# Optimization experiments

Measured on AMD Instinct MI355X. Metric: run time of the kernel, lower is better.

## Reference

```python
import jax, jax.numpy as jnp
import numpy as np

D_MODEL = 1024
D_STATE = 128
D_CONV = 4
EXPAND = 2
HEAD_DIM = 128
NGROUPS = 1
CHUNK = 256
D_INNER = EXPAND * D_MODEL          # 2048
HEADS = D_INNER // HEAD_DIM         # 16
D_IN_PROJ = 2 * D_INNER + 2 * NGROUPS * D_STATE + HEADS  # 4368
CONV_DIM = D_INNER + 2 * NGROUPS * D_STATE               # 2304
EPS = 1e-5


def setup_inputs() -> dict:
    key = jax.random.key(0)
    ks = jax.random.split(key, 10)
    B, L = 2, 2048
    u = jax.random.normal(ks[0], (B, L, D_MODEL), dtype=jnp.float32)
    in_proj_w = jax.random.normal(ks[1], (D_IN_PROJ, D_MODEL), dtype=jnp.float32) * 0.02
    conv_w = jax.random.normal(ks[2], (CONV_DIM, 1, D_CONV), dtype=jnp.float32) * 0.2
    conv_b = jnp.zeros((CONV_DIM,), dtype=jnp.float32)
    # dt_bias = inverse-softplus of dt sampled log-uniform in [dt_min, dt_max]
    dt = jnp.exp(jax.random.uniform(ks[3], (HEADS,)) * (np.log(0.1) - np.log(0.001)) + np.log(0.001))
    dt = jnp.clip(dt, 1e-4, None)
    dt_bias = (dt + jnp.log(-jnp.expm1(-dt))).astype(jnp.float32)
    A_log = jax.random.uniform(ks[4], (HEADS,), minval=np.log(0.001), maxval=np.log(0.999)).astype(jnp.float32)
    D_param = jax.random.uniform(ks[5], (HEADS,), minval=-0.5, maxval=0.5).astype(jnp.float32)
    norm_w = jnp.ones((D_INNER,), dtype=jnp.float32)
    out_proj_w = jax.random.normal(ks[6], (D_MODEL, D_INNER), dtype=jnp.float32) * 0.02
    out_proj_b = jnp.zeros((D_MODEL,), dtype=jnp.float32)
    return {"u": u, "in_proj_w": in_proj_w, "conv_w": conv_w, "conv_b": conv_b,
            "dt_bias": dt_bias, "A_log": A_log, "D_param": D_param,
            "norm_w": norm_w, "out_proj_w": out_proj_w, "out_proj_b": out_proj_b}


def _segsum_exp(a):
    # a: (..., T) -> exp of lower-triangular segment sums, (..., T, T)
    T = a.shape[-1]
    ac = jnp.cumsum(a, axis=-1)
    diff = ac[..., :, None] - ac[..., None, :]
    mask = jnp.tril(jnp.ones((T, T), dtype=bool))
    return jnp.where(mask, jnp.exp(jnp.where(mask, diff, 0.0)), 0.0)


def _ssd(xdt, dA, Bmat, Cmat):
    # xdt: (b,L,h,p) = x * dt ; dA: (b,L,h) = dt * A ; Bmat/Cmat: (b,L,n) (ngroups=1)
    b, L, h, p = xdt.shape
    nc, cs = L // CHUNK, CHUNK
    x_c = xdt.reshape(b, nc, cs, h, p)
    B_c = Bmat.reshape(b, nc, cs, -1)
    C_c = Cmat.reshape(b, nc, cs, -1)
    A_r = dA.reshape(b, nc, cs, h).transpose(0, 3, 1, 2)  # (b,h,nc,cs)
    Lmat = _segsum_exp(A_r)                               # (b,h,nc,cs,cs)
    Y_diag = jnp.einsum('bcin,bcjn,bhcij,bcjhp->bcihp', C_c, B_c, Lmat, x_c)
    A_cum = jnp.cumsum(A_r, axis=-1)                      # (b,h,nc,cs)
    decay_states = jnp.exp(A_cum[..., -1:] - A_cum)       # (b,h,nc,cs)
    states = jnp.einsum('bcin,bhci,bcihp->bchpn', B_c, decay_states, x_c)  # (b,nc,h,p,n)
    chunk_decay = jnp.exp(A_cum[..., -1])                 # (b,h,nc)

    def step(prev, inp):
        s, dec = inp  # s: (b,h,p,n), dec: (b,h)
        new = prev * dec[..., None, None] + s
        return new, prev  # emit state entering this chunk

    init = jnp.zeros((b, h, p, states.shape[-1]), dtype=xdt.dtype)
    _, prior = jax.lax.scan(step, init,
                            (states.transpose(1, 0, 2, 3, 4), chunk_decay.transpose(2, 0, 1)))
    prior = prior.transpose(1, 0, 2, 3, 4)                # (b,nc,h,p,n)
    state_decay_out = jnp.exp(A_cum)                      # (b,h,nc,cs)
    Y_off = jnp.einsum('bcin,bchpn,bhci->bcihp', C_c, prior, state_decay_out)
    return (Y_diag + Y_off).reshape(b, L, h, p)


def reference(u, in_proj_w, conv_w, conv_b, dt_bias, A_log, D_param, norm_w, out_proj_w, out_proj_b):
    b, L, _ = u.shape
    zxbcdt = u @ in_proj_w.T                              # (b,L,4368)
    z = zxbcdt[..., :D_INNER]
    xBC = zxbcdt[..., D_INNER:D_INNER + CONV_DIM]
    dt = zxbcdt[..., D_INNER + CONV_DIM:]                 # (b,L,H)
    dt = jax.nn.softplus(dt + dt_bias)
    # causal depthwise conv1d + SiLU
    xBC_t = xBC.transpose(0, 2, 1)                        # (b,C,L)
    xBC_t = jax.lax.conv_general_dilated(
        xBC_t, conv_w, window_strides=(1,), padding=[(D_CONV - 1, 0)],
        dimension_numbers=('NCH', 'OIH', 'NCH'), feature_group_count=CONV_DIM)
    xBC = jax.nn.silu(xBC_t.transpose(0, 2, 1) + conv_b)  # (b,L,C)
    x = xBC[..., :D_INNER].reshape(b, L, HEADS, HEAD_DIM)
    Bmat = xBC[..., D_INNER:D_INNER + NGROUPS * D_STATE]  # (b,L,n), ngroups=1
    Cmat = xBC[..., D_INNER + NGROUPS * D_STATE:]
    A = -jnp.exp(A_log)                                   # (H,)
    y = _ssd(x * dt[..., None], dt * A, Bmat, Cmat)
    y = y + D_param[None, None, :, None] * x              # skip connection
    y = y.reshape(b, L, D_INNER)
    # gated RMSNorm (norm_before_gate=False): normalize(y * silu(z)) * w
    y = y * jax.nn.silu(z)
    y = y * jax.lax.rsqrt(jnp.mean(y * y, axis=-1, keepdims=True) + EPS) * norm_w
    return y @ out_proj_w.T + out_proj_b
```

## Files before the change

kernel.cpp:

```cpp
#include <hip/hip_runtime.h>
#include <math.h>

#define B_N 2
#define L_N 2048
#define DM 1024
#define DIP 4368
#define DI 2048
#define CONVD 2304
#define NH 16
#define HD 128
#define NST 128
#define NC 8
#define CS 256
#define NROWS 4096

typedef __attribute__((ext_vector_type(8))) short short8;
typedef __attribute__((ext_vector_type(4))) float f32x4;

__device__ __forceinline__ float silu_f(float x) { return x / (1.f + expf(-x)); }

__device__ __forceinline__ unsigned short f2bf_rne(float x) {
  unsigned int u = __float_as_uint(x);
  u += 0x7FFFu + ((u >> 16) & 1u);
  return (unsigned short)(u >> 16);
}
__device__ __forceinline__ float bf2f(unsigned short h) {
  return __uint_as_float(((unsigned int)h) << 16);
}

template<int BIAS>
__global__ __launch_bounds__(256) void gemm_nt_mfma(const float* __restrict__ A,
                                                    const float* __restrict__ W,
                                                    const float* __restrict__ bias,
                                                    float* __restrict__ C,
                                                    int M, int N, int K) {
  __shared__ unsigned short Ah[4096], Al[4096], Bh[4096], Bl[4096];
  const int tid  = threadIdx.x;
  const int lane = tid & 63;
  const int wave = tid >> 6;
  const int wr = (wave & 1) * 64;
  const int wc = (wave >> 1) * 64;
  const int m0 = blockIdx.y * 128, n0 = blockIdx.x * 128;
  const int srow = tid >> 1;
  const int skh  = (tid & 1) * 16;
  const int skb0 = (tid & 1) * 2;
  const bool wvalid = (n0 + srow) < N;
  const float* Ap = A + (size_t)(m0 + srow) * K + skh;
  const float* Wp = W + (size_t)(n0 + srow) * K + skh;

  f32x4 acc[4][4] = {};

  const int ntiles = K >> 5;
  for (int kt = 0; kt < ntiles; ++kt) {
    const float* As = Ap + kt * 32;
    const float* Ws = Wp + kt * 32;
    float ab[16], wb[16];
    *(float4*)&ab[0]  = *(const float4*)(As + 0);
    *(float4*)&ab[4]  = *(const float4*)(As + 4);
    *(float4*)&ab[8]  = *(const float4*)(As + 8);
    *(float4*)&ab[12] = *(const float4*)(As + 12);
    if (wvalid) {
      *(float4*)&wb[0]  = *(const float4*)(Ws + 0);
      *(float4*)&wb[4]  = *(const float4*)(Ws + 4);
      *(float4*)&wb[8]  = *(const float4*)(Ws + 8);
      *(float4*)&wb[12] = *(const float4*)(Ws + 12);
    } else {
#pragma unroll
      for (int j = 0; j < 16; ++j) wb[j] = 0.f;
    }
    __syncthreads();
#pragma unroll
    for (int c = 0; c < 2; ++c) {
      const int kb = skb0 + c;
      const int off = (kb * 128 + srow) * 8;
      short8 hv, lv;
#pragma unroll
      for (int j = 0; j < 8; ++j) {
        float x = ab[c * 8 + j];
        unsigned short h = f2bf_rne(x);
        hv[j] = (short)h;
        lv[j] = (short)f2bf_rne(x - bf2f(h));
      }
      *(short8*)&Ah[off] = hv;
      *(short8*)&Al[off] = lv;
#pragma unroll
      for (int j = 0; j < 8; ++j) {
        float x = wb[c * 8 + j];
        unsigned short h = f2bf_rne(x);
        hv[j] = (short)h;
        lv[j] = (short)f2bf_rne(x - bf2f(h));
      }
      *(short8*)&Bh[off] = hv;
      *(short8*)&Bl[off] = lv;
    }
    __syncthreads();
    const int fra = ((lane >> 4) * 128 + wr + (lane & 15)) * 8;
    const int frb = ((lane >> 4) * 128 + wc + (lane & 15)) * 8;
    short8 ah[4], al[4];
#pragma unroll
    for (int mi = 0; mi < 4; ++mi) {
      ah[mi] = *(const short8*)&Ah[fra + mi * 128];
      al[mi] = *(const short8*)&Al[fra + mi * 128];
    }
#pragma unroll
    for (int ni = 0; ni < 4; ++ni) {
      short8 bh = *(const short8*)&Bh[frb + ni * 128];
      short8 bl = *(const short8*)&Bl[frb + ni * 128];
#pragma unroll
      for (int mi = 0; mi < 4; ++mi) {
        acc[mi][ni] = __builtin_amdgcn_mfma_f32_16x16x32_bf16(ah[mi], bh, acc[mi][ni], 0, 0, 0);
        acc[mi][ni] = __builtin_amdgcn_mfma_f32_16x16x32_bf16(ah[mi], bl, acc[mi][ni], 0, 0, 0);
        acc[mi][ni] = __builtin_amdgcn_mfma_f32_16x16x32_bf16(al[mi], bh, acc[mi][ni], 0, 0, 0);
      }
    }
  }
#pragma unroll
  for (int ni = 0; ni < 4; ++ni) {
    int gcolb = n0 + wc + ni * 16;
    if (gcolb >= N) continue;
    int gcol = gcolb + (lane & 15);
    float bv = BIAS ? bias[gcol] : 0.f;
#pragma unroll
    for (int mi = 0; mi < 4; ++mi) {
      int growb = m0 + wr + mi * 16 + (lane >> 4) * 4;
#pragma unroll
      for (int r = 0; r < 4; ++r) {
        C[(size_t)(growb + r) * N + gcol] = acc[mi][ni][r] + bv;
      }
    }
  }
}

__global__ __launch_bounds__(256) void conv_kernel(const float* __restrict__ zx,
                                                   const float* __restrict__ cw,
                                                   const float* __restrict__ cb,
                                                   float* __restrict__ xcout) {
  int c = blockIdx.x * 256 + threadIdx.x;
  int ml = blockIdx.y;
  int l = ml & (L_N - 1);
  const float* src = zx + (size_t)ml * DIP + DI + c;
  float w0 = cw[c * 4 + 0], w1 = cw[c * 4 + 1], w2 = cw[c * 4 + 2], w3 = cw[c * 4 + 3];
  float acc = cb[c] + w3 * src[0];
  if (l >= 1) acc += w2 * src[-(ptrdiff_t)DIP];
  if (l >= 2) acc += w1 * src[-2 * (ptrdiff_t)DIP];
  if (l >= 3) acc += w0 * src[-3 * (ptrdiff_t)DIP];
  xcout[(size_t)ml * CONVD + c] = silu_f(acc);
}

__global__ __launch_bounds__(256) void dtscan_kernel(const float* __restrict__ zx,
                                                     const float* __restrict__ dt_bias,
                                                     const float* __restrict__ A_log,
                                                     float* __restrict__ dts,
                                                     float* __restrict__ acum,
                                                     float* __restrict__ cdec) {
  int bch = blockIdx.x;
  int h = bch & 15, bc = bch >> 4;
  int i = threadIdx.x;
  int grow = bc * CS + i;
  float raw = zx[(size_t)grow * DIP + DI + CONVD + h] + dt_bias[h];
  float dt = raw > 20.f ? raw : log1pf(expf(raw));
  dts[grow * NH + h] = dt;
  float da = dt * (-expf(A_log[h]));
  __shared__ float sbuf[CS];
  sbuf[i] = da;
  __syncthreads();
  for (int off = 1; off < CS; off <<= 1) {
    float v = (i >= off) ? sbuf[i - off] : 0.f;
    __syncthreads();
    sbuf[i] += v;
    __syncthreads();
  }
  float ac = sbuf[i];
  acum[(size_t)bch * CS + i] = ac;
  if (i == CS - 1) cdec[bch] = expf(ac);
}

__global__ __launch_bounds__(256) void smat_kernel(const float* __restrict__ xc,
                                                   const float* __restrict__ acum,
                                                   float* __restrict__ S) {
  int t = blockIdx.x;
  int ti = 0, accn = 0;
  while (accn + ti + 1 <= t) { accn += ti + 1; ti++; }
  int tj = t - accn;
  int bc = blockIdx.y;
  int rowbase = bc * CS;
  int i0 = ti * 64, j0 = tj * 64;
  __shared__ float Cst[32][64];
  __shared__ float Bst[32][64];
  int tid = threadIdx.x, tx = tid & 15, ty = tid >> 4;
  float acc[4][4] = {};
  for (int kt = 0; kt < 4; ++kt) {
    int k0 = kt * 32;
    float4 cv[2], bv[2]; int rr[2], kk4[2];
#pragma unroll
    for (int rep = 0; rep < 2; ++rep) {
      int idx = rep * 256 + tid;
      rr[rep] = idx >> 3; kk4[rep] = (idx & 7) * 4;
      cv[rep] = *(const float4*)(xc + (size_t)(rowbase + i0 + rr[rep]) * CONVD + DI + NST + k0 + kk4[rep]);
      bv[rep] = *(const float4*)(xc + (size_t)(rowbase + j0 + rr[rep]) * CONVD + DI + k0 + kk4[rep]);
    }
    __syncthreads();
#pragma unroll
    for (int rep = 0; rep < 2; ++rep) {
      Cst[kk4[rep] + 0][rr[rep]] = cv[rep].x; Cst[kk4[rep] + 1][rr[rep]] = cv[rep].y;
      Cst[kk4[rep] + 2][rr[rep]] = cv[rep].z; Cst[kk4[rep] + 3][rr[rep]] = cv[rep].w;
      Bst[kk4[rep] + 0][rr[rep]] = bv[rep].x; Bst[kk4[rep] + 1][rr[rep]] = bv[rep].y;
      Bst[kk4[rep] + 2][rr[rep]] = bv[rep].z; Bst[kk4[rep] + 3][rr[rep]] = bv[rep].w;
    }
    __syncthreads();
#pragma unroll
    for (int kk = 0; kk < 32; ++kk) {
      float4 c4 = *(const float4*)&Cst[kk][ty * 4];
      float4 b4 = *(const float4*)&Bst[kk][tx * 4];
      float c[4] = {c4.x, c4.y, c4.z, c4.w};
      float b[4] = {b4.x, b4.y, b4.z, b4.w};
#pragma unroll
      for (int i = 0; i < 4; ++i)
#pragma unroll
        for (int j = 0; j < 4; ++j) acc[i][j] = fmaf(c[i], b[j], acc[i][j]);
    }
    __syncthreads();
  }
  const float* ac = acum + (size_t)bc * NH * CS;
  for (int h = 0; h < NH; ++h) {
    float ai[4], aj[4];
#pragma unroll
    for (int i = 0; i < 4; ++i) ai[i] = ac[h * CS + i0 + ty * 4 + i];
#pragma unroll
    for (int j = 0; j < 4; ++j) aj[j] = ac[h * CS + j0 + tx * 4 + j];
    float* Sp = S + ((size_t)bc * NH + h) * CS * CS;
#pragma unroll
    for (int i = 0; i < 4; ++i) {
      int gi = i0 + ty * 4 + i;
      float o[4];
#pragma unroll
      for (int j = 0; j < 4; ++j) {
        int gj = j0 + tx * 4 + j;
        o[j] = (gi >= gj) ? expf(ai[i] - aj[j]) * acc[i][j] : 0.f;
      }
      *(float4*)(Sp + (size_t)gi * CS + j0 + tx * 4) = make_float4(o[0], o[1], o[2], o[3]);
    }
  }
}

__global__ __launch_bounds__(256) void ydiag_kernel(const float* __restrict__ S,
                                                    const float* __restrict__ xc,
                                                    const float* __restrict__ dts,
                                                    const float* __restrict__ Dp,
                                                    float* __restrict__ Y) {
  int bch = blockIdx.y;
  int h = bch & 15, bc = bch >> 4;
  int i0 = blockIdx.x * 64;
  int rowbase = bc * CS;
  __shared__ float Sst[32][64];
  __shared__ float Xs[32][128];
  int tid = threadIdx.x, tx = tid & 15, ty = tid >> 4;
  float acc[4][8] = {};
  int ktiles = (blockIdx.x + 1) * 2;
  const float* Sbase = S + ((size_t)bch * CS + i0) * CS;
  for (int kt = 0; kt < ktiles; ++kt) {
    int k0 = kt * 32;
    float4 sv[2]; int sr[2], skq[2];
#pragma unroll
    for (int rep = 0; rep < 2; ++rep) {
      int idx = rep * 256 + tid;
      sr[rep] = idx >> 3; skq[rep] = (idx & 7) * 4;
      sv[rep] = *(const float4*)(Sbase + (size_t)sr[rep] * CS + k0 + skq[rep]);
    }
    float4 xv[4]; int jr[4], pq[4];
#pragma unroll
    for (int rep = 0; rep < 4; ++rep) {
      int idx = rep * 256 + tid;
      jr[rep] = idx >> 5; pq[rep] = (idx & 31) * 4;
      int grow = rowbase + k0 + jr[rep];
      float dtv = dts[grow * NH + h];
      float4 x4 = *(const float4*)(xc + (size_t)grow * CONVD + h * HD + pq[rep]);
      xv[rep] = make_float4(x4.x * dtv, x4.y * dtv, x4.z * dtv, x4.w * dtv);
    }
    __syncthreads();
#pragma unroll
    for (int rep = 0; rep < 2; ++rep) {
      Sst[skq[rep] + 0][sr[rep]] = sv[rep].x; Sst[skq[rep] + 1][sr[rep]] = sv[rep].y;
      Sst[skq[rep] + 2][sr[rep]] = sv[rep].z; Sst[skq[rep] + 3][sr[rep]] = sv[rep].w;
    }
#pragma unroll
    for (int rep = 0; rep < 4; ++rep) *(float4*)&Xs[jr[rep]][pq[rep]] = xv[rep];
    __syncthreads();
#pragma unroll
    for (int kk = 0; kk < 32; ++kk) {
      float4 s4 = *(const float4*)&Sst[kk][ty * 4];
      float4 x0 = *(const float4*)&Xs[kk][tx * 8];
      float4 x1 = *(const float4*)&Xs[kk][tx * 8 + 4];
      float s[4] = {s4.x, s4.y, s4.z, s4.w};
      float x8[8] = {x0.x, x0.y, x0.z, x0.w, x1.x, x1.y, x1.z, x1.w};
#pragma unroll
      for (int i = 0; i < 4; ++i)
#pragma unroll
        for (int j = 0; j < 8; ++j) acc[i][j] = fmaf(s[i], x8[j], acc[i][j]);
    }
    __syncthreads();
  }
  float Dv = Dp[h];
#pragma unroll
  for (int i = 0; i < 4; ++i) {
    int grow = rowbase + i0 + ty * 4 + i;
#pragma unroll
    for (int j = 0; j < 8; j += 4) {
      int p = tx * 8 + j;
      float4 x4 = *(const float4*)(xc + (size_t)grow * CONVD + h * HD + p);
      float4 v = make_float4(acc[i][j] + Dv * x4.x, acc[i][j + 1] + Dv * x4.y,
                             acc[i][j + 2] + Dv * x4.z, acc[i][j + 3] + Dv * x4.w);
      *(float4*)(Y + (size_t)grow * DI + h * HD + p) = v;
    }
  }
}

__global__ __launch_bounds__(256) void states_kernel(const float* __restrict__ xc,
                                                     const float* __restrict__ dts,
                                                     const float* __restrict__ acum,
                                                     float* __restrict__ st) {
  int bch = blockIdx.x;
  int h = bch & 15, bc = bch >> 4;
  int rowbase = bc * CS;
  __shared__ float Bs[32][128];
  __shared__ float Xs[32][128];
  int tid = threadIdx.x, tx = tid & 15, ty = tid >> 4;
  float acc[8][8] = {};
  const float* ac = acum + (size_t)bch * CS;
  float aclast = ac[CS - 1];
  for (int kt = 0; kt < 8; ++kt) {
    int k0 = kt * 32;
    float4 bv[4], xv[4]; int ir[4], q4[4];
#pragma unroll
    for (int rep = 0; rep < 4; ++rep) {
      int idx = rep * 256 + tid;
      ir[rep] = idx >> 5; q4[rep] = (idx & 31) * 4;
      int grow = rowbase + k0 + ir[rep];
      float dec = expf(aclast - ac[k0 + ir[rep]]);
      float4 b4 = *(const float4*)(xc + (size_t)grow * CONVD + DI + q4[rep]);
      bv[rep] = make_float4(b4.x * dec, b4.y * dec, b4.z * dec, b4.w * dec);
      float dtv = dts[grow * NH + h];
      float4 x4 = *(const float4*)(xc + (size_t)grow * CONVD + h * HD + q4[rep]);
      xv[rep] = make_float4(x4.x * dtv, x4.y * dtv, x4.z * dtv, x4.w * dtv);
    }
    __syncthreads();
#pragma unroll
    for (int rep = 0; rep < 4; ++rep) {
      *(float4*)&Bs[ir[rep]][q4[rep]] = bv[rep];
      *(float4*)&Xs[ir[rep]][q4[rep]] = xv[rep];
    }
    __syncthreads();
#pragma unroll
    for (int kk = 0; kk < 32; ++kk) {
      float4 b0 = *(const float4*)&Bs[kk][ty * 8];
      float4 b1 = *(const float4*)&Bs[kk][ty * 8 + 4];
      float4 x0 = *(const float4*)&Xs[kk][tx * 8];
      float4 x1 = *(const float4*)&Xs[kk][tx * 8 + 4];
      float bb[8] = {b0.x, b0.y, b0.z, b0.w, b1.x, b1.y, b1.z, b1.w};
      float xx[8] = {x0.x, x0.y, x0.z, x0.w, x1.x, x1.y, x1.z, x1.w};
#pragma unroll
      for (int i = 0; i < 8; ++i)
#pragma unroll
        for (int j = 0; j < 8; ++j) acc[i][j] = fmaf(bb[i], xx[j], acc[i][j]);
    }
    __syncthreads();
  }
#pragma unroll
  for (int i = 0; i < 8; ++i) {
    int n = ty * 8 + i;
#pragma unroll
    for (int j = 0; j < 8; j += 4) {
      int p = tx * 8 + j;
      float4 v = make_float4(acc[i][j], acc[i][j + 1], acc[i][j + 2], acc[i][j + 3]);
      *(float4*)(st + ((size_t)bch * NST + n) * HD + p) = v;
    }
  }
}

__global__ __launch_bounds__(256) void scan_kernel(const float* __restrict__ st,
                                                   const float* __restrict__ cdec,
                                                   float* __restrict__ pr) {
  int gid = blockIdx.x * 256 + threadIdx.x;
  int p = gid & 127;
  int n = (gid >> 7) & 127;
  int h = (gid >> 14) & 15;
  int b = gid >> 18;
  float state = 0.f;
  for (int c = 0; c < NC; ++c) {
    int bch = (b * NC + c) * NH + h;
    size_t idx = ((size_t)bch * NST + n) * HD + p;
    pr[idx] = state;
    state = state * cdec[bch] + st[idx];
  }
}

__global__ __launch_bounds__(256) void yoff_kernel(const float* __restrict__ xc,
                                                   const float* __restrict__ pr,
                                                   const float* __restrict__ acum,
                                                   float* __restrict__ Y) {
  int bch = blockIdx.y;
  int h = bch & 15, bc = bch >> 4;
  int i0 = blockIdx.x * 64;
  int rowbase = bc * CS;
  __shared__ float Cst[32][64];
  __shared__ float Ps[32][128];
  int tid = threadIdx.x, tx = tid & 15, ty = tid >> 4;
  float acc[4][8] = {};
  const float* Pbase = pr + (size_t)bch * NST * HD;
  for (int kt = 0; kt < 4; ++kt) {
    int k0 = kt * 32;
    float4 cv[2]; int rr[2], kq[2];
#pragma unroll
    for (int rep = 0; rep < 2; ++rep) {
      int idx = rep * 256 + tid;
      rr[rep] = idx >> 3; kq[rep] = (idx & 7) * 4;
      cv[rep] = *(const float4*)(xc + (size_t)(rowbase + i0 + rr[rep]) * CONVD + DI + NST + k0 + kq[rep]);
    }
    float4 pv[4]; int nr[4], pq[4];
#pragma unroll
    for (int rep = 0; rep < 4; ++rep) {
      int idx = rep * 256 + tid;
      nr[rep] = idx >> 5; pq[rep] = (idx & 31) * 4;
      pv[rep] = *(const float4*)(Pbase + (size_t)(k0 + nr[rep]) * HD + pq[rep]);
    }
    __syncthreads();
#pragma unroll
    for (int rep = 0; rep < 2; ++rep) {
      Cst[kq[rep] + 0][rr[rep]] = cv[rep].x; Cst[kq[rep] + 1][rr[rep]] = cv[rep].y;
      Cst[kq[rep] + 2][rr[rep]] = cv[rep].z; Cst[kq[rep] + 3][rr[rep]] = cv[rep].w;
    }
#pragma unroll
    for (int rep = 0; rep < 4; ++rep) *(float4*)&Ps[nr[rep]][pq[rep]] = pv[rep];
    __syncthreads();
#pragma unroll
    for (int kk = 0; kk < 32; ++kk) {
      float4 c4 = *(const float4*)&Cst[kk][ty * 4];
      float4 p0 = *(const float4*)&Ps[kk][tx * 8];
      float4 p1 = *(const float4*)&Ps[kk][tx * 8 + 4];
      float c[4] = {c4.x, c4.y, c4.z, c4.w};
      float p8[8] = {p0.x, p0.y, p0.z, p0.w, p1.x, p1.y, p1.z, p1.w};
#pragma unroll
      for (int i = 0; i < 4; ++i)
#pragma unroll
        for (int j = 0; j < 8; ++j) acc[i][j] = fmaf(c[i], p8[j], acc[i][j]);
    }
    __syncthreads();
  }
  const float* ac = acum + (size_t)bch * CS;
#pragma unroll
  for (int i = 0; i < 4; ++i) {
    int grow = rowbase + i0 + ty * 4 + i;
    float eai = expf(ac[i0 + ty * 4 + i]);
#pragma unroll
    for (int j = 0; j < 8; j += 4) {
      int p = tx * 8 + j;
      float4 y4 = *(const float4*)(Y + (size_t)grow * DI + h * HD + p);
      y4.x += eai * acc[i][j];     y4.y += eai * acc[i][j + 1];
      y4.z += eai * acc[i][j + 2]; y4.w += eai * acc[i][j + 3];
      *(float4*)(Y + (size_t)grow * DI + h * HD + p) = y4;
    }
  }
}

__global__ __launch_bounds__(256) void gnorm_kernel(const float* __restrict__ zx,
                                                    const float* __restrict__ nw,
                                                    float* __restrict__ Y) {
  int row = blockIdx.x;
  int tid = threadIdx.x;
  float vals[8];
  float ss = 0.f;
#pragma unroll
  for (int rep = 0; rep < 2; ++rep) {
    int c = tid * 8 + rep * 4;
    float4 yv = *(const float4*)(Y + (size_t)row * DI + c);
    float4 zv = *(const float4*)(zx + (size_t)row * DIP + c);
    float v0 = yv.x * silu_f(zv.x), v1 = yv.y * silu_f(zv.y);
    float v2 = yv.z * silu_f(zv.z), v3 = yv.w * silu_f(zv.w);
    vals[rep * 4 + 0] = v0; vals[rep * 4 + 1] = v1;
    vals[rep * 4 + 2] = v2; vals[rep * 4 + 3] = v3;
    ss += v0 * v0 + v1 * v1 + v2 * v2 + v3 * v3;
  }
  for (int off = 32; off > 0; off >>= 1) ss += __shfl_xor(ss, off);
  __shared__ float wsum[4];
  if ((tid & 63) == 0) wsum[tid >> 6] = ss;
  __syncthreads();
  float scale = rsqrtf((wsum[0] + wsum[1] + wsum[2] + wsum[3]) * (1.f / DI) + 1e-5f);
#pragma unroll
  for (int rep = 0; rep < 2; ++rep) {
    int c = tid * 8 + rep * 4;
    float4 w4 = *(const float4*)(nw + c);
    float4 o = make_float4(vals[rep * 4 + 0] * scale * w4.x, vals[rep * 4 + 1] * scale * w4.y,
                           vals[rep * 4 + 2] * scale * w4.z, vals[rep * 4 + 3] * scale * w4.w);
    *(float4*)(Y + (size_t)row * DI + c) = o;
  }
}

extern "C" void kernel_launch(void* const* d_in, const int* in_sizes, int n_in,
                              void* d_out, int out_size, void* d_ws, size_t ws_size,
                              hipStream_t stream) {
  const float* u          = (const float*)d_in[0];
  const float* in_proj_w  = (const float*)d_in[1];
  const float* conv_w     = (const float*)d_in[2];
  const float* conv_b     = (const float*)d_in[3];
  const float* dt_bias    = (const float*)d_in[4];
  const float* A_log      = (const float*)d_in[5];
  const float* D_param    = (const float*)d_in[6];
  const float* norm_w     = (const float*)d_in[7];
  const float* out_proj_w = (const float*)d_in[8];
  const float* out_proj_b = (const float*)d_in[9];
  float* out = (float*)d_out;
  float* ws  = (float*)d_ws;

  const size_t off_zx = 0;
  const size_t off_xc = off_zx + (size_t)NROWS * DIP;
  const size_t off_dt = off_xc + (size_t)NROWS * CONVD;
  const size_t off_ac = off_dt + (size_t)NROWS * NH;
  const size_t off_cd = off_ac + (size_t)B_N * NC * NH * CS;
  const size_t off_S  = off_cd + 256;
  const size_t off_st = off_S  + (size_t)B_N * NC * NH * CS * CS;
  const size_t off_pr = off_st + (size_t)B_N * NC * NH * NST * HD;
  const size_t off_Y  = off_pr + (size_t)B_N * NC * NH * NST * HD;
  const size_t total  = off_Y  + (size_t)NROWS * DI;
  if (ws_size < total * sizeof(float)) return;

  float* zx   = ws + off_zx;
  float* xc   = ws + off_xc;
  float* dts  = ws + off_dt;
  float* acum = ws + off_ac;
  float* cdec = ws + off_cd;
  float* S    = ws + off_S;
  float* st   = ws + off_st;
  float* pr   = ws + off_pr;
  float* Y    = ws + off_Y;

  gemm_nt_mfma<0><<<dim3(35, 32), 256, 0, stream>>>(u, in_proj_w, nullptr, zx, NROWS, DIP, DM);
  conv_kernel<<<dim3(9, NROWS), 256, 0, stream>>>(zx, conv_w, conv_b, xc);
  dtscan_kernel<<<256, 256, 0, stream>>>(zx, dt_bias, A_log, dts, acum, cdec);
  smat_kernel<<<dim3(10, 16), 256, 0, stream>>>(xc, acum, S);
  ydiag_kernel<<<dim3(4, 256), 256, 0, stream>>>(S, xc, dts, D_param, Y);
  states_kernel<<<256, 256, 0, stream>>>(xc, dts, acum, st);
  scan_kernel<<<2048, 256, 0, stream>>>(st, cdec, pr);
  yoff_kernel<<<dim3(4, 256), 256, 0, stream>>>(xc, pr, acum, Y);
  gnorm_kernel<<<NROWS, 256, 0, stream>>>(zx, norm_w, Y);
  gemm_nt_mfma<1><<<dim3(8, 32), 256, 0, stream>>>(Y, out_proj_w, out_proj_b, out, NROWS, DM, DI);
}
```

Baseline: 618.8 us.

## Pre-split GEMM operands to bf16 hi/lo and fuse ydiag with yoff

After: 645.9 us. 1.04x slower.

```diff
diff --git a/kernel.cpp b/kernel.cpp
--- a/kernel.cpp
+++ b/kernel.cpp
@@ -14,6 +14,12 @@
 #define CS 256
 #define NROWS 4096
 
+#define NU   4194304
+#define NWI  4472832
+#define NWIP 4587520
+#define NWO  2097152
+#define NY   8388608
+
 typedef __attribute__((ext_vector_type(8))) short short8;
 typedef __attribute__((ext_vector_type(4))) float f32x4;
 
@@ -28,12 +34,45 @@
   return __uint_as_float(((unsigned int)h) << 16);
 }
 
+__device__ __forceinline__ void gload16(const unsigned short* g, unsigned short* lds) {
+  __builtin_amdgcn_global_load_lds((const __attribute__((address_space(1))) void*)g,
+                                   (__attribute__((address_space(3))) void*)lds, 16, 0, 0);
+}
+
+__global__ __launch_bounds__(256) void split_kernel(const float* __restrict__ src,
+                                                    unsigned short* __restrict__ hi,
+                                                    unsigned short* __restrict__ lo,
+                                                    int n, int npad) {
+  int stride = gridDim.x * 256;
+  for (int i4 = blockIdx.x * 256 + threadIdx.x; i4 < (npad >> 2); i4 += stride) {
+    int base = i4 * 4;
+    float v[4];
+    if (base + 3 < n) {
+      float4 t = *(const float4*)(src + base);
+      v[0] = t.x; v[1] = t.y; v[2] = t.z; v[3] = t.w;
+    } else {
+#pragma unroll
+      for (int j = 0; j < 4; ++j) v[j] = (base + j < n) ? src[base + j] : 0.f;
+    }
+    ushort4 hv, lv;
+    unsigned short h;
+    h = f2bf_rne(v[0]); hv.x = h; lv.x = f2bf_rne(v[0] - bf2f(h));
+    h = f2bf_rne(v[1]); hv.y = h; lv.y = f2bf_rne(v[1] - bf2f(h));
+    h = f2bf_rne(v[2]); hv.z = h; lv.z = f2bf_rne(v[2] - bf2f(h));
+    h = f2bf_rne(v[3]); hv.w = h; lv.w = f2bf_rne(v[3] - bf2f(h));
+    *(ushort4*)(hi + base) = hv;
+    *(ushort4*)(lo + base) = lv;
+  }
+}
+
 template<int BIAS>
-__global__ __launch_bounds__(256) void gemm_nt_mfma(const float* __restrict__ A,
-                                                    const float* __restrict__ W,
-                                                    const float* __restrict__ bias,
-                                                    float* __restrict__ C,
-                                                    int M, int N, int K) {
+__global__ __launch_bounds__(256) void gemm_bf16split(const unsigned short* __restrict__ Ahg,
+                                                      const unsigned short* __restrict__ Alg,
+                                                      const unsigned short* __restrict__ Whg,
+                                                      const unsigned short* __restrict__ Wlg,
+                                                      const float* __restrict__ bias,
+                                                      float* __restrict__ C,
+                                                      int M, int N, int K) {
   __shared__ unsigned short Ah[4096], Al[4096], Bh[4096], Bl[4096];
   const int tid  = threadIdx.x;
   const int lane = tid & 63;
@@ -41,57 +80,27 @@
   const int wr = (wave & 1) * 64;
   const int wc = (wave >> 1) * 64;
   const int m0 = blockIdx.y * 128, n0 = blockIdx.x * 128;
-  const int srow = tid >> 1;
-  const int skh  = (tid & 1) * 16;
-  const int skb0 = (tid & 1) * 2;
-  const bool wvalid = (n0 + srow) < N;
-  const float* Ap = A + (size_t)(m0 + srow) * K + skh;
-  const float* Wp = W + (size_t)(n0 + srow) * K + skh;
+
+  int srow[2], skb[2], loff[2];
+#pragma unroll
+  for (int r = 0; r < 2; ++r) {
+    int idx = (wave * 2 + r) * 64 + lane;
+    skb[r]  = idx >> 7;
+    srow[r] = idx & 127;
+    loff[r] = (wave * 2 + r) * 512;
+  }
 
   f32x4 acc[4][4] = {};
-
   const int ntiles = K >> 5;
   for (int kt = 0; kt < ntiles; ++kt) {
-    const float* As = Ap + kt * 32;
-    const float* Ws = Wp + kt * 32;
-    float ab[16], wb[16];
-    *(float4*)&ab[0]  = *(const float4*)(As + 0);
-    *(float4*)&ab[4]  = *(const float4*)(As + 4);
-    *(float4*)&ab[8]  = *(const float4*)(As + 8);
-    *(float4*)&ab[12] = *(const float4*)(As + 12);
-    if (wvalid) {
-      *(float4*)&wb[0]  = *(const float4*)(Ws + 0);
-      *(float4*)&wb[4]  = *(const float4*)(Ws + 4);
-      *(float4*)&wb[8]  = *(const float4*)(Ws + 8);
-      *(float4*)&wb[12] = *(const float4*)(Ws + 12);
-    } else {
-#pragma unroll
-      for (int j = 0; j < 16; ++j) wb[j] = 0.f;
-    }
-    __syncthreads();
-#pragma unroll
-    for (int c = 0; c < 2; ++c) {
-      const int kb = skb0 + c;
-      const int off = (kb * 128 + srow) * 8;
-      short8 hv, lv;
-#pragma unroll
-      for (int j = 0; j < 8; ++j) {
-        float x = ab[c * 8 + j];
-        unsigned short h = f2bf_rne(x);
-        hv[j] = (short)h;
-        lv[j] = (short)f2bf_rne(x - bf2f(h));
-      }
-      *(short8*)&Ah[off] = hv;
-      *(short8*)&Al[off] = lv;
-#pragma unroll
-      for (int j = 0; j < 8; ++j) {
-        float x = wb[c * 8 + j];
-        unsigned short h = f2bf_rne(x);
-        hv[j] = (short)h;
-        lv[j] = (short)f2bf_rne(x - bf2f(h));
-      }
-      *(short8*)&Bh[off] = hv;
-      *(short8*)&Bl[off] = lv;
+#pragma unroll
+    for (int r = 0; r < 2; ++r) {
+      size_t ga = (size_t)(m0 + srow[r]) * K + kt * 32 + skb[r] * 8;
+      size_t gw = (size_t)(n0 + srow[r]) * K + kt * 32 + skb[r] * 8;
+      gload16(Ahg + ga, &Ah[loff[r]]);
+      gload16(Alg + ga, &Al[loff[r]]);
+      gload16(Whg + gw, &Bh[loff[r]]);
+      gload16(Wlg + gw, &Bl[loff[r]]);
     }
     __syncthreads();
     const int fra = ((lane >> 4) * 128 + wr + (lane & 15)) * 8;
@@ -113,6 +122,7 @@
         acc[mi][ni] = __builtin_amdgcn_mfma_f32_16x16x32_bf16(al[mi], bh, acc[mi][ni], 0, 0, 0);
       }
     }
+    __syncthreads();
   }
 #pragma unroll
   for (int ni = 0; ni < 4; ++ni) {
@@ -243,11 +253,13 @@
   }
 }
 
-__global__ __launch_bounds__(256) void ydiag_kernel(const float* __restrict__ S,
-                                                    const float* __restrict__ xc,
-                                                    const float* __restrict__ dts,
-                                                    const float* __restrict__ Dp,
-                                                    float* __restrict__ Y) {
+__global__ __launch_bounds__(256) void ydiag_yoff_kernel(const float* __restrict__ S,
+                                                         const float* __restrict__ xc,
+                                                         const float* __restrict__ dts,
+                                                         const float* __restrict__ pr,
+                                                         const float* __restrict__ acum,
+                                                         const float* __restrict__ Dp,
+                                                         float* __restrict__ Y) {
   int bch = blockIdx.y;
   int h = bch & 15, bc = bch >> 4;
   int i0 = blockIdx.x * 64;
@@ -256,6 +268,7 @@
   __shared__ float Xs[32][128];
   int tid = threadIdx.x, tx = tid & 15, ty = tid >> 4;
   float acc[4][8] = {};
+  float acc2[4][8] = {};
   int ktiles = (blockIdx.x + 1) * 2;
   const float* Sbase = S + ((size_t)bch * CS + i0) * CS;
   for (int kt = 0; kt < ktiles; ++kt) {
@@ -300,16 +313,60 @@
     }
     __syncthreads();
   }
+  const float* Pbase = pr + (size_t)bch * NST * HD;
+  for (int kt = 0; kt < 4; ++kt) {
+    int k0 = kt * 32;
+    float4 cv[2]; int rr[2], kq[2];
+#pragma unroll
+    for (int rep = 0; rep < 2; ++rep) {
+      int idx = rep * 256 + tid;
+      rr[rep] = idx >> 3; kq[rep] = (idx & 7) * 4;
+      cv[rep] = *(const float4*)(xc + (size_t)(rowbase + i0 + rr[rep]) * CONVD + DI + NST + k0 + kq[rep]);
+    }
+    float4 pv[4]; int nr[4], pq[4];
+#pragma unroll
+    for (int rep = 0; rep < 4; ++rep) {
+      int idx = rep * 256 + tid;
+      nr[rep] = idx >> 5; pq[rep] = (idx & 31) * 4;
+      pv[rep] = *(const float4*)(Pbase + (size_t)(k0 + nr[rep]) * HD + pq[rep]);
+    }
+    __syncthreads();
+#pragma unroll
+    for (int rep = 0; rep < 2; ++rep) {
+      Sst[kq[rep] + 0][rr[rep]] = cv[rep].x; Sst[kq[rep] + 1][rr[rep]] = cv[rep].y;
+      Sst[kq[rep] + 2][rr[rep]] = cv[rep].z; Sst[kq[rep] + 3][rr[rep]] = cv[rep].w;
+    }
+#pragma unroll
+    for (int rep = 0; rep < 4; ++rep) *(float4*)&Xs[nr[rep]][pq[rep]] = pv[rep];
+    __syncthreads();
+#pragma unroll
+    for (int kk = 0; kk < 32; ++kk) {
+      float4 c4 = *(const float4*)&Sst[kk][ty * 4];
+      float4 p0 = *(const float4*)&Xs[kk][tx * 8];
+      float4 p1 = *(const float4*)&Xs[kk][tx * 8 + 4];
+      float c[4] = {c4.x, c4.y, c4.z, c4.w};
+      float p8[8] = {p0.x, p0.y, p0.z, p0.w, p1.x, p1.y, p1.z, p1.w};
+#pragma unroll
+      for (int i = 0; i < 4; ++i)
+#pragma unroll
+        for (int j = 0; j < 8; ++j) acc2[i][j] = fmaf(c[i], p8[j], acc2[i][j]);
+    }
+    __syncthreads();
+  }
+  const float* ac = acum + (size_t)bch * CS;
   float Dv = Dp[h];
 #pragma unroll
   for (int i = 0; i < 4; ++i) {
     int grow = rowbase + i0 + ty * 4 + i;
+    float eai = expf(ac[i0 + ty * 4 + i]);
 #pragma unroll
     for (int j = 0; j < 8; j += 4) {
       int p = tx * 8 + j;
       float4 x4 = *(const float4*)(xc + (size_t)grow * CONVD + h * HD + p);
-      float4 v = make_float4(acc[i][j] + Dv * x4.x, acc[i][j + 1] + Dv * x4.y,
-                             acc[i][j + 2] + Dv * x4.z, acc[i][j + 3] + Dv * x4.w);
+      float4 v = make_float4(acc[i][j + 0] + eai * acc2[i][j + 0] + Dv * x4.x,
+                             acc[i][j + 1] + eai * acc2[i][j + 1] + Dv * x4.y,
+                             acc[i][j + 2] + eai * acc2[i][j + 2] + Dv * x4.z,
+                             acc[i][j + 3] + eai * acc2[i][j + 3] + Dv * x4.w);
       *(float4*)(Y + (size_t)grow * DI + h * HD + p) = v;
     }
   }
@@ -394,77 +451,11 @@
   }
 }
 
-__global__ __launch_bounds__(256) void yoff_kernel(const float* __restrict__ xc,
-                                                   const float* __restrict__ pr,
-                                                   const float* __restrict__ acum,
-                                                   float* __restrict__ Y) {
-  int bch = blockIdx.y;
-  int h = bch & 15, bc = bch >> 4;
-  int i0 = blockIdx.x * 64;
-  int rowbase = bc * CS;
-  __shared__ float Cst[32][64];
-  __shared__ float Ps[32][128];
-  int tid = threadIdx.x, tx = tid & 15, ty = tid >> 4;
-  float acc[4][8] = {};
-  const float* Pbase = pr + (size_t)bch * NST * HD;
-  for (int kt = 0; kt < 4; ++kt) {
-    int k0 = kt * 32;
-    float4 cv[2]; int rr[2], kq[2];
-#pragma unroll
-    for (int rep = 0; rep < 2; ++rep) {
-      int idx = rep * 256 + tid;
-      rr[rep] = idx >> 3; kq[rep] = (idx & 7) * 4;
-      cv[rep] = *(const float4*)(xc + (size_t)(rowbase + i0 + rr[rep]) * CONVD + DI + NST + k0 + kq[rep]);
-    }
-    float4 pv[4]; int nr[4], pq[4];
-#pragma unroll
-    for (int rep = 0; rep < 4; ++rep) {
-      int idx = rep * 256 + tid;
-      nr[rep] = idx >> 5; pq[rep] = (idx & 31) * 4;
-      pv[rep] = *(const float4*)(Pbase + (size_t)(k0 + nr[rep]) * HD + pq[rep]);
-    }
-    __syncthreads();
-#pragma unroll
-    for (int rep = 0; rep < 2; ++rep) {
-      Cst[kq[rep] + 0][rr[rep]] = cv[rep].x; Cst[kq[rep] + 1][rr[rep]] = cv[rep].y;
-      Cst[kq[rep] + 2][rr[rep]] = cv[rep].z; Cst[kq[rep] + 3][rr[rep]] = cv[rep].w;
-    }
-#pragma unroll
-    for (int rep = 0; rep < 4; ++rep) *(float4*)&Ps[nr[rep]][pq[rep]] = pv[rep];
-    __syncthreads();
-#pragma unroll
-    for (int kk = 0; kk < 32; ++kk) {
-      float4 c4 = *(const float4*)&Cst[kk][ty * 4];
-      float4 p0 = *(const float4*)&Ps[kk][tx * 8];
-      float4 p1 = *(const float4*)&Ps[kk][tx * 8 + 4];
-      float c[4] = {c4.x, c4.y, c4.z, c4.w};
-      float p8[8] = {p0.x, p0.y, p0.z, p0.w, p1.x, p1.y, p1.z, p1.w};
-#pragma unroll
-      for (int i = 0; i < 4; ++i)
-#pragma unroll
-        for (int j = 0; j < 8; ++j) acc[i][j] = fmaf(c[i], p8[j], acc[i][j]);
-    }
-    __syncthreads();
-  }
-  const float* ac = acum + (size_t)bch * CS;
-#pragma unroll
-  for (int i = 0; i < 4; ++i) {
-    int grow = rowbase + i0 + ty * 4 + i;
-    float eai = expf(ac[i0 + ty * 4 + i]);
-#pragma unroll
-    for (int j = 0; j < 8; j += 4) {
-      int p = tx * 8 + j;
-      float4 y4 = *(const float4*)(Y + (size_t)grow * DI + h * HD + p);
-      y4.x += eai * acc[i][j];     y4.y += eai * acc[i][j + 1];
-      y4.z += eai * acc[i][j + 2]; y4.w += eai * acc[i][j + 3];
-      *(float4*)(Y + (size_t)grow * DI + h * HD + p) = y4;
-    }
-  }
-}
-
-__global__ __launch_bounds__(256) void gnorm_kernel(const float* __restrict__ zx,
-                                                    const float* __restrict__ nw,
-                                                    float* __restrict__ Y) {
+__global__ __launch_bounds__(256) void gnorm_split_kernel(const float* __restrict__ zx,
+                                                          const float* __restrict__ nw,
+                                                          const float* __restrict__ Yin,
+                                                          unsigned short* __restrict__ yh,
+                                                          unsigned short* __restrict__ yl) {
   int row = blockIdx.x;
   int tid = threadIdx.x;
   float vals[8];
@@ -472,7 +463,7 @@
 #pragma unroll
   for (int rep = 0; rep < 2; ++rep) {
     int c = tid * 8 + rep * 4;
-    float4 yv = *(const float4*)(Y + (size_t)row * DI + c);
+    float4 yv = *(const float4*)(Yin + (size_t)row * DI + c);
     float4 zv = *(const float4*)(zx + (size_t)row * DIP + c);
     float v0 = yv.x * silu_f(zv.x), v1 = yv.y * silu_f(zv.y);
     float v2 = yv.z * silu_f(zv.z), v3 = yv.w * silu_f(zv.w);
@@ -485,14 +476,22 @@
   if ((tid & 63) == 0) wsum[tid >> 6] = ss;
   __syncthreads();
   float scale = rsqrtf((wsum[0] + wsum[1] + wsum[2] + wsum[3]) * (1.f / DI) + 1e-5f);
+  short8 hv, lv;
 #pragma unroll
   for (int rep = 0; rep < 2; ++rep) {
     int c = tid * 8 + rep * 4;
     float4 w4 = *(const float4*)(nw + c);
-    float4 o = make_float4(vals[rep * 4 + 0] * scale * w4.x, vals[rep * 4 + 1] * scale * w4.y,
-                           vals[rep * 4 + 2] * scale * w4.z, vals[rep * 4 + 3] * scale * w4.w);
-    *(float4*)(Y + (size_t)row * DI + c) = o;
-  }
+    float o[4] = {vals[rep * 4 + 0] * scale * w4.x, vals[rep * 4 + 1] * scale * w4.y,
+                  vals[rep * 4 + 2] * scale * w4.z, vals[rep * 4 + 3] * scale * w4.w};
+#pragma unroll
+    for (int q = 0; q < 4; ++q) {
+      unsigned short h = f2bf_rne(o[q]);
+      hv[rep * 4 + q] = (short)h;
+      lv[rep * 4 + q] = (short)f2bf_rne(o[q] - bf2f(h));
+    }
+  }
+  *(short8*)(yh + (size_t)row * DI + tid * 8) = hv;
+  *(short8*)(yl + (size_t)row * DI + tid * 8) = lv;
 }
 
 extern "C" void kernel_launch(void* const* d_in, const int* in_sizes, int n_in,
@@ -533,14 +532,25 @@
   float* pr   = ws + off_pr;
   float* Y    = ws + off_Y;
 
-  gemm_nt_mfma<0><<<dim3(35, 32), 256, 0, stream>>>(u, in_proj_w, nullptr, zx, NROWS, DIP, DM);
+  unsigned short* uh  = (unsigned short*)S;
+  unsigned short* ul  = uh  + NU;
+  unsigned short* wih = ul  + NU;
+  unsigned short* wil = wih + NWIP;
+  unsigned short* woh = (unsigned short*)st;
+  unsigned short* wol = woh + NWO;
+  unsigned short* yh  = (unsigned short*)S;
+  unsigned short* yl  = yh + NY;
+
+  split_kernel<<<2048, 256, 0, stream>>>(u, uh, ul, NU, NU);
+  split_kernel<<<2048, 256, 0, stream>>>(in_proj_w, wih, wil, NWI, NWIP);
+  gemm_bf16split<0><<<dim3(35, 32), 256, 0, stream>>>(uh, ul, wih, wil, nullptr, zx, NROWS, DIP, DM);
   conv_kernel<<<dim3(9, NROWS), 256, 0, stream>>>(zx, conv_w, conv_b, xc);
   dtscan_kernel<<<256, 256, 0, stream>>>(zx, dt_bias, A_log, dts, acum, cdec);
-  smat_kernel<<<dim3(10, 16), 256, 0, stream>>>(xc, acum, S);
-  ydiag_kernel<<<dim3(4, 256), 256, 0, stream>>>(S, xc, dts, D_param, Y);
   states_kernel<<<256, 256, 0, stream>>>(xc, dts, acum, st);
   scan_kernel<<<2048, 256, 0, stream>>>(st, cdec, pr);
-  yoff_kernel<<<dim3(4, 256), 256, 0, stream>>>(xc, pr, acum, Y);
-  gnorm_kernel<<<NROWS, 256, 0, stream>>>(zx, norm_w, Y);
-  gemm_nt_mfma<1><<<dim3(8, 32), 256, 0, stream>>>(Y, out_proj_w, out_proj_b, out, NROWS, DM, DI);
-}
+  split_kernel<<<2048, 256, 0, stream>>>(out_proj_w, woh, wol, NWO, NWO);
+  smat_kernel<<<dim3(10, 16), 256, 0, stream>>>(xc, acum, S);
+  ydiag_yoff_kernel<<<dim3(4, 256), 256, 0, stream>>>(S, xc, dts, pr, acum, D_param, Y);
+  gnorm_split_kernel<<<NROWS, 256, 0, stream>>>(zx, norm_w, Y, yh, yl);
+  gemm_bf16split<1><<<dim3(8, 32), 256, 0, stream>>>(yh, yl, woh, wol, out_proj_b, out, NROWS, DM, DI);
+}
```
